# Kernel optimization log

Measured on AMD Instinct MI355X. Metric: run time of the kernel, lower is better.

## Reference

```python
import jax, jax.numpy as jnp
import numpy as np

D_MODEL = 1024
D_STATE = 16
D_CONV = 4
EXPAND = 2
D_INNER = EXPAND * D_MODEL          # 2048
DT_RANK = (D_MODEL + 15) // 16      # 64
B_SZ, SEQ = 2, 1024
LN_EPS = 1e-6


def setup_inputs() -> dict:
    key = jax.random.key(0)
    ks = jax.random.split(key, 12)
    s = 0.02
    x = jax.random.normal(ks[0], (B_SZ, SEQ, D_MODEL), dtype=jnp.float32)
    W_in = jax.random.normal(ks[1], (D_MODEL, 2 * D_INNER), dtype=jnp.float32) * s
    conv_w = jax.random.normal(ks[2], (D_INNER, D_CONV), dtype=jnp.float32) * s
    conv_b = jnp.zeros((D_INNER,), dtype=jnp.float32)
    W_xproj = jax.random.normal(ks[3], (D_INNER, DT_RANK + 2 * D_STATE), dtype=jnp.float32) * s
    W_dt = jax.random.normal(ks[4], (DT_RANK, D_INNER), dtype=jnp.float32) * (DT_RANK ** -0.5)
    # dt bias ~ log-uniform init as in Mamba (softplus^-1 of dt in [1e-3, 1e-1])
    dt = jnp.exp(jax.random.uniform(ks[5], (D_INNER,)) * (np.log(0.1) - np.log(1e-3)) + np.log(1e-3))
    b_dt = dt + jnp.log(-jnp.expm1(-dt))  # inverse softplus
    A_log = jnp.log(jnp.broadcast_to(jnp.arange(1, D_STATE + 1, dtype=jnp.float32), (D_INNER, D_STATE)))
    D_param = jnp.ones((D_INNER,), dtype=jnp.float32)
    W_out = jax.random.normal(ks[6], (D_INNER, D_MODEL), dtype=jnp.float32) * s
    gamma = jnp.ones((D_MODEL,), dtype=jnp.float32)
    beta = jnp.zeros((D_MODEL,), dtype=jnp.float32)
    return {"x": x, "W_in": W_in, "conv_w": conv_w, "conv_b": conv_b,
            "W_xproj": W_xproj, "W_dt": W_dt, "b_dt": b_dt, "A_log": A_log,
            "D_param": D_param, "W_out": W_out, "gamma": gamma, "beta": beta}


def _mamba(x, W_in, conv_w, conv_b, W_xproj, W_dt, b_dt, A_log, D_param, W_out):
    B, L, _ = x.shape
    xz = x @ W_in                                  # [B,L,2*d_inner]
    xi, z = jnp.split(xz, 2, axis=-1)              # [B,L,d_inner] each
    # causal depthwise conv1d, kernel D_CONV
    xp = jnp.pad(xi, ((0, 0), (D_CONV - 1, 0), (0, 0)))
    xc = conv_b
    for k in range(D_CONV):
        xc = xc + xp[:, k:k + L, :] * conv_w[:, k]
    xc = jax.nn.silu(xc)                           # [B,L,d_inner]
    x_dbl = xc @ W_xproj                           # [B,L,dt_rank+2*d_state]
    dt_r = x_dbl[..., :DT_RANK]
    B_ssm = x_dbl[..., DT_RANK:DT_RANK + D_STATE]  # [B,L,d_state]
    C_ssm = x_dbl[..., DT_RANK + D_STATE:]         # [B,L,d_state]
    dt = jax.nn.softplus(dt_r @ W_dt + b_dt)       # [B,L,d_inner]
    A = -jnp.exp(A_log)                            # [d_inner,d_state]
    dA = jnp.exp(dt[..., None] * A)                # [B,L,d_inner,d_state]
    dBu = dt[..., None] * B_ssm[:, :, None, :] * xc[..., None]
    # selective scan over time (time-major for lax.scan)
    dA_t = jnp.moveaxis(dA, 1, 0)                  # [L,B,d_inner,d_state]
    dBu_t = jnp.moveaxis(dBu, 1, 0)
    C_t = jnp.moveaxis(C_ssm, 1, 0)                # [L,B,d_state]
    h0 = jnp.zeros((B, D_INNER, D_STATE), dtype=x.dtype)

    def step(h, inp):
        a, bu, c = inp
        h = a * h + bu
        y = jnp.einsum('bdn,bn->bd', h, c)
        return h, y

    _, ys = jax.lax.scan(step, h0, (dA_t, dBu_t, C_t))
    y = jnp.moveaxis(ys, 0, 1)                     # [B,L,d_inner]
    y = y + xc * D_param
    y = y * jax.nn.silu(z)
    return y @ W_out                               # [B,L,d_model]


def reference(x, W_in, conv_w, conv_b, W_xproj, W_dt, b_dt, A_log, D_param, W_out, gamma, beta):
    m = _mamba(x, W_in, conv_w, conv_b, W_xproj, W_dt, b_dt, A_log, D_param, W_out)
    mu = jnp.mean(m, axis=-1, keepdims=True)
    var = jnp.mean(jnp.square(m - mu), axis=-1, keepdims=True)
    ln = (m - mu) * jax.lax.rsqrt(var + LN_EPS) * gamma + beta
    return x + ln
```

## Files before the change

### kernel.cpp

```cpp
#include <hip/hip_runtime.h>
#include <math.h>

#define DM   1024
#define DI   2048
#define DS   16
#define DTR  64
#define NB   2
#define SEQL 1024
#define NTOK (NB*SEQL)
#define XND  96
#define XNP  128
#define CK   128
#define CL   8
#define NPART 2

typedef __bf16 bf16x8 __attribute__((ext_vector_type(8)));
typedef __bf16 bf16x4 __attribute__((ext_vector_type(4)));
typedef float  f32x4  __attribute__((ext_vector_type(4)));

#define PREP_BLOCKS 3872

__device__ inline void trans_tile64(const float* __restrict__ W,
                                    __bf16* __restrict__ WT, int K, int N,
                                    int n0, int k0, int tid, __bf16 (*t)[65])
{
    const int tx = tid & 63, ty = tid >> 6;
    #pragma unroll
    for (int i = 0; i < 16; i++)
        t[ty * 16 + i][tx] = (__bf16)W[(size_t)(k0 + ty * 16 + i) * N + n0 + tx];
    __syncthreads();
    #pragma unroll
    for (int i = 0; i < 16; i++)
        WT[(size_t)(n0 + ty * 16 + i) * K + k0 + tx] = t[tx][ty * 16 + i];
}

__global__ __launch_bounds__(256) void prep(
    const float* __restrict__ x, const float* __restrict__ W_in,
    const float* __restrict__ W_out, const float* __restrict__ W_dt,
    const float* __restrict__ W_xprj,
    __bf16* __restrict__ xb, __bf16* __restrict__ W_inT,
    __bf16* __restrict__ W_outT, __bf16* __restrict__ WdtT,
    __bf16* __restrict__ W_xprT, float* __restrict__ xdbl)
{
    __shared__ __bf16 t[64][65];
    int bid = blockIdx.x;
    const int tid = threadIdx.x;

    if (bid < 256) {
        const int i = bid * 1024 + tid * 4;
        const float4 z = {0.f, 0.f, 0.f, 0.f};
        *reinterpret_cast<float4*>(&xdbl[i]) = z;
        return;
    }
    bid -= 256;
    if (bid < 1024) {
        const int e = (bid * 256 + tid) * 8;
        const float4 v0 = *reinterpret_cast<const float4*>(&x[e]);
        const float4 v1 = *reinterpret_cast<const float4*>(&x[e + 4]);
        bf16x8 o;
        o[0] = (__bf16)v0.x; o[1] = (__bf16)v0.y; o[2] = (__bf16)v0.z; o[3] = (__bf16)v0.w;
        o[4] = (__bf16)v1.x; o[5] = (__bf16)v1.y; o[6] = (__bf16)v1.z; o[7] = (__bf16)v1.w;
        *reinterpret_cast<bf16x8*>(&xb[e]) = o;
        return;
    }
    bid -= 1024;
    if (bid < 1024) {
        trans_tile64(W_in, W_inT, DM, 2 * DI, (bid & 63) * 64, (bid >> 6) * 64, tid, t);
        return;
    }
    bid -= 1024;
    if (bid < 512) {
        trans_tile64(W_out, W_outT, DI, DM, (bid & 15) * 64, (bid >> 4) * 64, tid, t);
        return;
    }
    bid -= 512;
    if (bid < 32) {
        trans_tile64(W_dt, WdtT, DTR, DI, bid * 64, 0, tid, t);
        return;
    }
    bid -= 32;
    {
        const int idx = bid * 256 + tid;
        const int k = idx & (DI - 1);
        const int n = idx >> 11;
        W_xprT[(size_t)n * DI + k] = (n < XND) ? (__bf16)W_xprj[(size_t)k * XND + n]
                                               : (__bf16)0.f;
    }
}

template<int MODE, int SWZ, int TN>
__global__ __launch_bounds__(256) void gemm_bf16(
    const __bf16* __restrict__ A, const __bf16* __restrict__ Bt,
    void* __restrict__ Cp, int M, int N, int K, int ldc,
    const float* __restrict__ bias)
{
    constexpr int NFR = TN / 32;
    constexpr bool PIPE = (MODE != 2);
    constexpr int ASZ = 128 * 64, BSZ = TN * 64;
    constexpr int STG = (PIPE ? 2 : 1) * (ASZ + BSZ);
    constexpr int SMEM = (STG > 128 * TN) ? STG : 128 * TN;
    __shared__ __bf16 smem[SMEM];
    const int tid  = threadIdx.x;
    const int lane = tid & 63;
    const int wid  = tid >> 6;
    const int wr   = wid >> 1, wc = wid & 1;

    int bx = blockIdx.x, by = blockIdx.y;
    if (SWZ == 1 || SWZ == 2) {
        const int gx = gridDim.x, gy = gridDim.y;
        const int nxy = gx * gy;
        const int q = nxy >> 3;
        int lin = by * gx + bx;
        lin = (lin & 7) * q + (lin >> 3);
        if (SWZ == 1) { by = lin / gx; bx = lin % gx; }
        else          { bx = lin / gy; by = lin % gy; }
    } else if (SWZ == 3) {
        const int lin = by * gridDim.x + bx;
        const int r   = lin & 7;
        const int idx = lin >> 3;
        bx = (r & 3) * 8 + (idx & 7);
        by = (r >> 2) * 8 + (idx >> 3);
    }
    const int brow = by * 128, bcol = bx * TN;
    const int kper = K / gridDim.z;
    const int kbeg = blockIdx.z * kper, kend = kbeg + kper;

    f32x4 acc[4][NFR] = {};

    auto stage = [&](int buf, int k0) {
        __bf16* As = smem + buf * (ASZ + BSZ);
        __bf16* Bs = As + ASZ;
        if (MODE == 2) {
            const float* Af = reinterpret_cast<const float*>(A);
            #pragma unroll
            for (int p = 0; p < 4; p++) {
                const int i = p * 256 + tid;
                const int r = i >> 3;
                const int j = i & 7;
                const float4 v0 = *reinterpret_cast<const float4*>(
                    &Af[(size_t)(brow + r) * XNP + j * 8]);
                const float4 v1 = *reinterpret_cast<const float4*>(
                    &Af[(size_t)(brow + r) * XNP + j * 8 + 4]);
                bf16x8 o;
                o[0] = (__bf16)v0.x; o[1] = (__bf16)v0.y; o[2] = (__bf16)v0.z; o[3] = (__bf16)v0.w;
                o[4] = (__bf16)v1.x; o[5] = (__bf16)v1.y; o[6] = (__bf16)v1.z; o[7] = (__bf16)v1.w;
                *reinterpret_cast<bf16x8*>(&As[r * 64 + ((j ^ (r & 7))) * 8]) = o;
            }
        } else {
            #pragma unroll
            for (int p = 0; p < 4; p++) {
                const int i = p * 256 + tid;
                const int r = i >> 3;
                const int gc = ((i & 7) ^ (r & 7)) * 8;
                __builtin_amdgcn_global_load_lds(
                    (const __attribute__((address_space(1))) void*)(A + (size_t)(brow + r) * K + k0 + gc),
                    (__attribute__((address_space(3))) void*)(&As[i * 8]), 16, 0, 0);
            }
        }
        #pragma unroll
        for (int p = 0; p < TN / 32; p++) {
            const int i = p * 256 + tid;
            const int r = i >> 3;
            const int gc = ((i & 7) ^ (r & 7)) * 8;
            __builtin_amdgcn_global_load_lds(
                (const __attribute__((address_space(1))) void*)(Bt + (size_t)(bcol + r) * K + k0 + gc),
                (__attribute__((address_space(3))) void*)(&Bs[i * 8]), 16, 0, 0);
        }
    };

    auto compute = [&](int buf) {
        const __bf16* As = smem + buf * (ASZ + BSZ);
        const __bf16* Bs = As + ASZ;
        bf16x8 a[2][4], b[2][NFR];
        const int rA = wr * 64 + (lane & 15);
        const int rB = wc * (TN / 2) + (lane & 15);
        const int cq = lane >> 4;
        const int rx = lane & 7;
        #pragma unroll
        for (int ks = 0; ks < 2; ks++) {
            const int sl = ((ks * 4 + cq) ^ rx) * 8;
            #pragma unroll
            for (int m = 0; m < 4; m++)
                a[ks][m] = *reinterpret_cast<const bf16x8*>(&As[(rA + m * 16) * 64 + sl]);
            #pragma unroll
            for (int n = 0; n < NFR; n++)
                b[ks][n] = *reinterpret_cast<const bf16x8*>(&Bs[(rB + n * 16) * 64 + sl]);
        }
        __builtin_amdgcn_s_setprio(1);
        #pragma unroll
        for (int ks = 0; ks < 2; ks++)
            #pragma unroll
            for (int m = 0; m < 4; m++)
                #pragma unroll
                for (int n = 0; n < NFR; n++)
                    acc[m][n] = __builtin_amdgcn_mfma_f32_16x16x32_bf16(
                        a[ks][m], b[ks][n], acc[m][n], 0, 0, 0);
        __builtin_amdgcn_s_setprio(0);
    };

    const int nt = (kend - kbeg) >> 6;
    if constexpr (PIPE) {
        constexpr int LOADS = 4 + TN / 32;
        stage(0, kbeg);
        int cur = 0;
        for (int t = 0; t < nt; t++) {
            if (t + 1 < nt) {
                stage(cur ^ 1, kbeg + ((t + 1) << 6));
                asm volatile("s_waitcnt vmcnt(%0)" :: "n"(LOADS) : "memory");
            } else {
                asm volatile("s_waitcnt vmcnt(0)" ::: "memory");
            }
            __builtin_amdgcn_s_barrier();
            __builtin_amdgcn_sched_barrier(0);
            compute(cur);
            __builtin_amdgcn_sched_barrier(0);
            __builtin_amdgcn_s_barrier();
            cur ^= 1;
        }
    } else {
        for (int k0 = kbeg; k0 < kend; k0 += 64) {
            __syncthreads();
            stage(0, k0);
            __syncthreads();
            compute(0);
        }
    }

    const int crl = wr * 64 + (lane >> 4) * 4;
    const int ccl = wc * (TN / 2) + (lane & 15);

    if (MODE == 1) {
        #pragma unroll
        for (int m = 0; m < 4; m++)
            #pragma unroll
            for (int n = 0; n < NFR; n++) {
                const int col = bcol + ccl + n * 16;
                #pragma unroll
                for (int j = 0; j < 4; j++)
                    atomicAdd(&((float*)Cp)[(size_t)(brow + crl + m * 16 + j) * ldc + col],
                              acc[m][n][j]);
            }
    } else {
        __syncthreads();
        __bf16* Cs = smem;
        #pragma unroll
        for (int m = 0; m < 4; m++)
            #pragma unroll
            for (int n = 0; n < NFR; n++) {
                #pragma unroll
                for (int j = 0; j < 4; j++) {
                    float v = acc[m][n][j];
                    if (MODE == 2) {
                        v += bias[bcol + ccl + n * 16];
                        v = fmaxf(v, 0.f) + log1pf(__expf(-fabsf(v)));
                    }
                    Cs[(crl + m * 16 + j) * TN + ccl + n * 16] = (__bf16)v;
                }
            }
        __syncthreads();
        __bf16* Cb = (__bf16*)Cp +
            (size_t)blockIdx.z * ((MODE == 3) ? (size_t)M * ldc : 0);
        constexpr int CHUNKS = 128 * TN / 8;
        #pragma unroll
        for (int p = 0; p < CHUNKS / 256; p++) {
            const int i = p * 256 + tid;
            const int r = i / (TN / 8);
            const int cc = (i % (TN / 8)) * 8;
            *reinterpret_cast<bf16x8*>(&Cb[(size_t)(brow + r) * ldc + bcol + cc]) =
                *reinterpret_cast<const bf16x8*>(&Cs[r * TN + cc]);
        }
    }
}

__global__ __launch_bounds__(256) void conv_silu(
    const __bf16* __restrict__ xzb, const float* __restrict__ conv_w,
    const float* __restrict__ conv_b, __bf16* __restrict__ xcb)
{
    const int q  = gridDim.x >> 3;
    const int sb = (blockIdx.x & 7) * q + (blockIdx.x >> 3);
    const int g  = sb * 256 + threadIdx.x;
    const int d0 = (g & 255) * 8;
    const int tok = g >> 8;
    const int t   = tok & (SEQL - 1);

    float4 wv[8];
    #pragma unroll
    for (int j = 0; j < 8; j++)
        wv[j] = *reinterpret_cast<const float4*>(&conv_w[(d0 + j) * 4]);
    float acc[8];
    {
        const float4 b0 = *reinterpret_cast<const float4*>(&conv_b[d0]);
        const float4 b1 = *reinterpret_cast<const float4*>(&conv_b[d0 + 4]);
        acc[0] = b0.x; acc[1] = b0.y; acc[2] = b0.z; acc[3] = b0.w;
        acc[4] = b1.x; acc[5] = b1.y; acc[6] = b1.z; acc[7] = b1.w;
    }
    #pragma unroll
    for (int k = 0; k < 4; k++) {
        const int tt = t + k - 3;
        if (tt >= 0) {
            const bf16x8 v = *reinterpret_cast<const bf16x8*>(
                &xzb[(size_t)(tok + k - 3) * (2 * DI) + d0]);
            #pragma unroll
            for (int j = 0; j < 8; j++) {
                const float wk = (k == 0) ? wv[j].x : (k == 1) ? wv[j].y
                               : (k == 2) ? wv[j].z : wv[j].w;
                acc[j] += (float)v[j] * wk;
            }
        }
    }
    bf16x8 o;
    #pragma unroll
    for (int j = 0; j < 8; j++) {
        const float a = acc[j];
        o[j] = (__bf16)(a / (1.f + __expf(-a)));
    }
    *reinterpret_cast<bf16x8*>(&xcb[(size_t)g * 8]) = o;
}

__global__ __launch_bounds__(256) void scan_partial(
    const __bf16* __restrict__ xcb, const float* __restrict__ xdbl,
    const __bf16* __restrict__ dtb, const float* __restrict__ A_log,
    __bf16* __restrict__ hpart, float* __restrict__ sdtb)
{
    __shared__ float Bsh[CL][16];
    const int tid = threadIdx.x;
    const int d = blockIdx.x * 256 + tid;
    const int c = blockIdx.y, b = blockIdx.z;
    const size_t base = (size_t)b * SEQL + c * CL;
    {
        const int st = tid >> 4, sg = tid & 15;
        if (st < CL) Bsh[st][sg] = xdbl[(base + st) * XNP + DTR + sg];
    }
    float dtv[CL], xcv[CL];
    #pragma unroll
    for (int t = 0; t < CL; t++) {
        dtv[t] = (float)dtb[(base + t) * DI + d];
        xcv[t] = (float)xcb[(base + t) * DI + d];
    }
    float Av[16];
    #pragma unroll
    for (int i = 0; i < 4; i++) {
        const float4 v = *reinterpret_cast<const float4*>(&A_log[(size_t)d * 16 + i * 4]);
        Av[i*4+0] = -__expf(v.x); Av[i*4+1] = -__expf(v.y);
        Av[i*4+2] = -__expf(v.z); Av[i*4+3] = -__expf(v.w);
    }
    __syncthreads();
    float h[16] = {};
    float sdt = 0.f;
    #pragma unroll
    for (int t = 0; t < CL; t++) {
        sdt += dtv[t];
        const float dx = dtv[t] * xcv[t];
        #pragma unroll
        for (int n = 0; n < 16; n++)
            h[n] = __expf(dtv[t] * Av[n]) * h[n] + dx * Bsh[t][n];
    }
    const size_t ob = ((size_t)(b * CK + c) * DI + d) * 16;
    bf16x8 o0, o1;
    #pragma unroll
    for (int i = 0; i < 8; i++) { o0[i] = (__bf16)h[i]; o1[i] = (__bf16)h[i + 8]; }
    *reinterpret_cast<bf16x8*>(&hpart[ob])     = o0;
    *reinterpret_cast<bf16x8*>(&hpart[ob + 8]) = o1;
    sdtb[(size_t)(b * CK + c) * DI + d] = sdt;
}

__global__ __launch_bounds__(256) void scan_combine(
    const float* __restrict__ A_log, const float* __restrict__ sdtb,
    const __bf16* __restrict__ hpart, __bf16* __restrict__ hentry)
{
    const int idx = blockIdx.x * 256 + threadIdx.x;
    const int n = idx & 15;
    const int d = (idx >> 4) & (DI - 1);
    const int b = idx >> 15;
    const float A = -__expf(A_log[(size_t)d * 16 + n]);
    float h = 0.f;
    for (int cb = 0; cb < CK / 16; cb++) {
        float hl[16], sv[16];
        #pragma unroll
        for (int j = 0; j < 16; j++) {
            const int c = cb * 16 + j;
            hl[j] = (float)hpart[((size_t)(b * CK + c) * DI + d) * 16 + n];
            sv[j] = sdtb[(size_t)(b * CK + c) * DI + d];
        }
        #pragma unroll
        for (int j = 0; j < 16; j++) {
            const int c = cb * 16 + j;
            hentry[((size_t)(b * CK + c) * DI + d) * 16 + n] = (__bf16)h;
            h = __expf(A * sv[j]) * h + hl[j];
        }
    }
}

__global__ __launch_bounds__(256) void scan_final(
    const __bf16* __restrict__ xzb, const __bf16* __restrict__ xcb,
    const float* __restrict__ xdbl, const __bf16* __restrict__ dtb,
    const float* __restrict__ A_log, const float* __restrict__ Dp,
    const __bf16* __restrict__ hentry, __bf16* __restrict__ yb)
{
    __shared__ float Bsh[CL][16];
    __shared__ float Csh[CL][16];
    const int tid = threadIdx.x;
    const int d = blockIdx.x * 256 + tid;
    const int c = blockIdx.y, b = blockIdx.z;
    const size_t base = (size_t)b * SEQL + c * CL;
    {
        const int st = tid >> 4, sg = tid & 15;
        if (st < CL)
            Bsh[st][sg] = xdbl[(base + st) * XNP + DTR + sg];
        else if (st < 2 * CL)
            Csh[st - CL][sg] = xdbl[(base + st - CL) * XNP + DTR + DS + sg];
    }
    float dtv[CL], xcv[CL], zv[CL];
    #pragma unroll
    for (int t = 0; t < CL; t++) {
        dtv[t] = (float)dtb[(base + t) * DI + d];
        xcv[t] = (float)xcb[(base + t) * DI + d];
        zv[t]  = (float)xzb[(base + t) * (2 * DI) + DI + d];
    }
    float Av[16];
    #pragma unroll
    for (int i = 0; i < 4; i++) {
        const float4 v = *reinterpret_cast<const float4*>(&A_log[(size_t)d * 16 + i * 4]);
        Av[i*4+0] = -__expf(v.x); Av[i*4+1] = -__expf(v.y);
        Av[i*4+2] = -__expf(v.z); Av[i*4+3] = -__expf(v.w);
    }
    float h[16];
    const size_t ob = ((size_t)(b * CK + c) * DI + d) * 16;
    {
        const bf16x8 v0 = *reinterpret_cast<const bf16x8*>(&hentry[ob]);
        const bf16x8 v1 = *reinterpret_cast<const bf16x8*>(&hentry[ob + 8]);
        #pragma unroll
        for (int i = 0; i < 8; i++) { h[i] = (float)v0[i]; h[i + 8] = (float)v1[i]; }
    }
    const float Dv = Dp[d];
    __syncthreads();
    #pragma unroll
    for (int t = 0; t < CL; t++) {
        const float dx = dtv[t] * xcv[t];
        float y = 0.f;
        #pragma unroll
        for (int n = 0; n < 16; n++) {
            h[n] = __expf(dtv[t] * Av[n]) * h[n] + dx * Bsh[t][n];
            y += h[n] * Csh[t][n];
        }
        y += xcv[t] * Dv;
        y *= zv[t] / (1.f + __expf(-zv[t]));
        yb[(base + t) * DI + d] = (__bf16)y;
    }
}

__global__ __launch_bounds__(256) void ln_add(
    const float* __restrict__ x, const __bf16* __restrict__ mpart,
    const float* __restrict__ gamma, const float* __restrict__ beta,
    float* __restrict__ out)
{
    const int tok = blockIdx.x;
    const int tid = threadIdx.x;
    const int lane = tid & 63, wave = tid >> 6;
    __shared__ float red1[4], red2[4];
    __shared__ float stats[2];

    float4 v = {0.f, 0.f, 0.f, 0.f};
    #pragma unroll
    for (int p = 0; p < NPART; p++) {
        const bf16x4 mv = *reinterpret_cast<const bf16x4*>(
            &mpart[((size_t)p * NTOK + tok) * DM + tid * 4]);
        v.x += (float)mv[0]; v.y += (float)mv[1];
        v.z += (float)mv[2]; v.w += (float)mv[3];
    }
    float s1 = v.x + v.y + v.z + v.w;
    float s2 = v.x * v.x + v.y * v.y + v.z * v.z + v.w * v.w;
    #pragma unroll
    for (int o = 32; o > 0; o >>= 1) {
        s1 += __shfl_down(s1, o, 64);
        s2 += __shfl_down(s2, o, 64);
    }
    if (lane == 0) { red1[wave] = s1; red2[wave] = s2; }
    __syncthreads();
    if (tid == 0) {
        const float m1 = (red1[0] + red1[1] + red1[2] + red1[3]) * (1.f / DM);
        const float m2 = (red2[0] + red2[1] + red2[2] + red2[3]) * (1.f / DM);
        stats[0] = m1;
        stats[1] = rsqrtf(fmaxf(m2 - m1 * m1, 0.f) + 1e-6f);
    }
    __syncthreads();
    const float mu = stats[0];
    const float rs = stats[1];

    const float4 g  = reinterpret_cast<const float4*>(gamma)[tid];
    const float4 bb = reinterpret_cast<const float4*>(beta)[tid];
    const float4 xv = reinterpret_cast<const float4*>(&x[(size_t)tok * DM])[tid];
    float4 o;
    o.x = xv.x + (v.x - mu) * rs * g.x + bb.x;
    o.y = xv.y + (v.y - mu) * rs * g.y + bb.y;
    o.z = xv.z + (v.z - mu) * rs * g.z + bb.z;
    o.w = xv.w + (v.w - mu) * rs * g.w + bb.w;
    reinterpret_cast<float4*>(&out[(size_t)tok * DM])[tid] = o;
}

extern "C" void kernel_launch(void* const* d_in, const int* in_sizes, int n_in,
                              void* d_out, int out_size, void* d_ws, size_t ws_size,
                              hipStream_t stream)
{
    const float* x      = (const float*)d_in[0];
    const float* W_in   = (const float*)d_in[1];
    const float* conv_w = (const float*)d_in[2];
    const float* conv_b = (const float*)d_in[3];
    const float* W_xprj = (const float*)d_in[4];
    const float* W_dt   = (const float*)d_in[5];
    const float* b_dt   = (const float*)d_in[6];
    const float* A_log  = (const float*)d_in[7];
    const float* D_par  = (const float*)d_in[8];
    const float* W_out  = (const float*)d_in[9];
    const float* gamma  = (const float*)d_in[10];
    const float* beta   = (const float*)d_in[11];
    float* out = (float*)d_out;

    char* w = (char*)d_ws;
    __bf16* xzb    = (__bf16*)(w + 0);
    __bf16* xcb    = (__bf16*)(w + 16777216);
    float*  xdbl   = (float*) (w + 25165824);
    __bf16* dtb    = (__bf16*)(w + 26214400);
    __bf16* mpart  = (__bf16*)(w + 34603008);
    __bf16* hpart  = (__bf16*)(w + 51380224);
    __bf16* hentry = (__bf16*)(w + 68157440);
    float*  sdtb   = (float*) (w + 84934656);
    __bf16* xb     = (__bf16*)(w + 87031808);
    __bf16* W_inT  = (__bf16*)(w + 91226112);
    __bf16* W_outT = (__bf16*)(w + 99614720);
    __bf16* W_xprT = (__bf16*)(w + 103809024);
    __bf16* WdtT   = (__bf16*)(w + 104333312);
    __bf16* yb     = (__bf16*)(w + 104595456);

    prep<<<PREP_BLOCKS, 256, 0, stream>>>(
        x, W_in, W_out, W_dt, W_xprj, xb, W_inT, W_outT, WdtT, W_xprT, xdbl);

    gemm_bf16<3, 3, 128><<<dim3(32, 16, 1), 256, 0, stream>>>(
        xb, W_inT, xzb, NTOK, 2 * DI, DM, 2 * DI, nullptr);

    conv_silu<<<(NTOK * DI / 8) / 256, 256, 0, stream>>>(xzb, conv_w, conv_b, xcb);

    gemm_bf16<1, 0, 128><<<dim3(1, 16, 16), 256, 0, stream>>>(
        xcb, W_xprT, xdbl, NTOK, XNP, DI, XNP, nullptr);

    gemm_bf16<2, 0, 64><<<dim3(32, 16, 1), 256, 0, stream>>>(
        (const __bf16*)xdbl, WdtT, dtb, NTOK, DI, DTR, DI, b_dt);

    scan_partial<<<dim3(DI / 256, CK, NB), 256, 0, stream>>>(
        xcb, xdbl, dtb, A_log, hpart, sdtb);
    scan_combine<<<NB * DI * DS / 256, 256, 0, stream>>>(A_log, sdtb, hpart, hentry);
    scan_final<<<dim3(DI / 256, CK, NB), 256, 0, stream>>>(
        xzb, xcb, xdbl, dtb, A_log, D_par, hentry, yb);

    gemm_bf16<3, 1, 128><<<dim3(8, 16, NPART), 256, 0, stream>>>(
        yb, W_outT, mpart, NTOK, DM, DI, DM, nullptr);

    ln_add<<<NTOK, 256, 0, stream>>>(x, mpart, gamma, beta, out);
}
```

Before: 148.6 us.

## Fuse dt projection and softplus into scan kernels, drop separate dt GEMM

Removes the dedicated dt_proj GEMM (MODE 2) that wrote a bf16 dt tensor, and instead recomputes dt per token inside both scan_partial and scan_final. Each thread loads its 64-wide W_dt row into registers, the block stages the dt_rank slice of x_dbl into shared memory, and a 64-term dot product plus softplus runs inline. This removes one launch and the write and re-read of a [tokens, d_inner] dt tensor. The cost is the dt projection being done twice on CUDA cores instead of once on MFMA, plus extra register pressure.

```diff
diff --git a/kernel.cpp b/kernel.cpp
--- a/kernel.cpp
+++ b/kernel.cpp
@@ -95,9 +95,8 @@
     const float* __restrict__ bias)
 {
     constexpr int NFR = TN / 32;
-    constexpr bool PIPE = (MODE != 2);
     constexpr int ASZ = 128 * 64, BSZ = TN * 64;
-    constexpr int STG = (PIPE ? 2 : 1) * (ASZ + BSZ);
+    constexpr int STG = 2 * (ASZ + BSZ);
     constexpr int SMEM = (STG > 128 * TN) ? STG : 128 * TN;
     __shared__ __bf16 smem[SMEM];
     const int tid  = threadIdx.x;
@@ -130,32 +129,14 @@
     auto stage = [&](int buf, int k0) {
         __bf16* As = smem + buf * (ASZ + BSZ);
         __bf16* Bs = As + ASZ;
-        if (MODE == 2) {
-            const float* Af = reinterpret_cast<const float*>(A);
-            #pragma unroll
-            for (int p = 0; p < 4; p++) {
-                const int i = p * 256 + tid;
-                const int r = i >> 3;
-                const int j = i & 7;
-                const float4 v0 = *reinterpret_cast<const float4*>(
-                    &Af[(size_t)(brow + r) * XNP + j * 8]);
-                const float4 v1 = *reinterpret_cast<const float4*>(
-                    &Af[(size_t)(brow + r) * XNP + j * 8 + 4]);
-                bf16x8 o;
-                o[0] = (__bf16)v0.x; o[1] = (__bf16)v0.y; o[2] = (__bf16)v0.z; o[3] = (__bf16)v0.w;
-                o[4] = (__bf16)v1.x; o[5] = (__bf16)v1.y; o[6] = (__bf16)v1.z; o[7] = (__bf16)v1.w;
-                *reinterpret_cast<bf16x8*>(&As[r * 64 + ((j ^ (r & 7))) * 8]) = o;
-            }
-        } else {
-            #pragma unroll
-            for (int p = 0; p < 4; p++) {
-                const int i = p * 256 + tid;
-                const int r = i >> 3;
-                const int gc = ((i & 7) ^ (r & 7)) * 8;
-                __builtin_amdgcn_global_load_lds(
-                    (const __attribute__((address_space(1))) void*)(A + (size_t)(brow + r) * K + k0 + gc),
-                    (__attribute__((address_space(3))) void*)(&As[i * 8]), 16, 0, 0);
-            }
+        #pragma unroll
+        for (int p = 0; p < 4; p++) {
+            const int i = p * 256 + tid;
+            const int r = i >> 3;
+            const int gc = ((i & 7) ^ (r & 7)) * 8;
+            __builtin_amdgcn_global_load_lds(
+                (const __attribute__((address_space(1))) void*)(A + (size_t)(brow + r) * K + k0 + gc),
+                (__attribute__((address_space(3))) void*)(&As[i * 8]), 16, 0, 0);
         }
         #pragma unroll
         for (int p = 0; p < TN / 32; p++) {
@@ -199,7 +180,7 @@
     };
 
     const int nt = (kend - kbeg) >> 6;
-    if constexpr (PIPE) {
+    {
         constexpr int LOADS = 4 + TN / 32;
         stage(0, kbeg);
         int cur = 0;
@@ -217,13 +198,6 @@
             __builtin_amdgcn_s_barrier();
             cur ^= 1;
         }
-    } else {
-        for (int k0 = kbeg; k0 < kend; k0 += 64) {
-            __syncthreads();
-            stage(0, k0);
-            __syncthreads();
-            compute(0);
-        }
     }
 
     const int crl = wr * 64 + (lane >> 4) * 4;
@@ -246,20 +220,12 @@
         #pragma unroll
         for (int m = 0; m < 4; m++)
             #pragma unroll
-            for (int n = 0; n < NFR; n++) {
+            for (int n = 0; n < NFR; n++)
                 #pragma unroll
-                for (int j = 0; j < 4; j++) {
-                    float v = acc[m][n][j];
-                    if (MODE == 2) {
-                        v += bias[bcol + ccl + n * 16];
-                        v = fmaxf(v, 0.f) + log1pf(__expf(-fabsf(v)));
-                    }
-                    Cs[(crl + m * 16 + j) * TN + ccl + n * 16] = (__bf16)v;
-                }
-            }
+                for (int j = 0; j < 4; j++)
+                    Cs[(crl + m * 16 + j) * TN + ccl + n * 16] = (__bf16)acc[m][n][j];
         __syncthreads();
-        __bf16* Cb = (__bf16*)Cp +
-            (size_t)blockIdx.z * ((MODE == 3) ? (size_t)M * ldc : 0);
+        __bf16* Cb = (__bf16*)Cp + (size_t)blockIdx.z * (size_t)M * ldc;
         constexpr int CHUNKS = 128 * TN / 8;
         #pragma unroll
         for (int p = 0; p < CHUNKS / 256; p++) {
@@ -317,12 +283,35 @@
     *reinterpret_cast<bf16x8*>(&xcb[(size_t)g * 8]) = o;
 }
 
+__device__ inline void stage_dtr(const float* __restrict__ xdbl,
+                                 size_t base, int tid, float (*Rsh)[64])
+{
+    const int rr = tid >> 5;
+    const int rc = (tid & 31) * 2;
+    const float2 rv = *reinterpret_cast<const float2*>(&xdbl[(base + rr) * XNP + rc]);
+    Rsh[rr][rc] = rv.x; Rsh[rr][rc + 1] = rv.y;
+}
+
+__device__ inline float dt_dot(const float (*Rsh)[64], int t,
+                               const bf16x8* wv, float bdt)
+{
+    float dot = bdt;
+    #pragma unroll
+    for (int i = 0; i < 8; i++)
+        #pragma unroll
+        for (int j = 0; j < 8; j++)
+            dot += Rsh[t][i * 8 + j] * (float)wv[i][j];
+    return fmaxf(dot, 0.f) + log1pf(__expf(-fabsf(dot)));
+}
+
 __global__ __launch_bounds__(256) void scan_partial(
     const __bf16* __restrict__ xcb, const float* __restrict__ xdbl,
-    const __bf16* __restrict__ dtb, const float* __restrict__ A_log,
+    const __bf16* __restrict__ WdtT, const float* __restrict__ b_dt,
+    const float* __restrict__ A_log,
     __bf16* __restrict__ hpart, float* __restrict__ sdtb)
 {
     __shared__ float Bsh[CL][16];
+    __shared__ float Rsh[CL][64];
     const int tid = threadIdx.x;
     const int d = blockIdx.x * 256 + tid;
     const int c = blockIdx.y, b = blockIdx.z;
@@ -330,13 +319,17 @@
     {
         const int st = tid >> 4, sg = tid & 15;
         if (st < CL) Bsh[st][sg] = xdbl[(base + st) * XNP + DTR + sg];
-    }
-    float dtv[CL], xcv[CL];
-    #pragma unroll
-    for (int t = 0; t < CL; t++) {
-        dtv[t] = (float)dtb[(base + t) * DI + d];
+        stage_dtr(xdbl, base, tid, Rsh);
+    }
+    bf16x8 wv[8];
+    #pragma unroll
+    for (int i = 0; i < 8; i++)
+        wv[i] = *reinterpret_cast<const bf16x8*>(&WdtT[(size_t)d * DTR + i * 8]);
+    const float bdt = b_dt[d];
+    float xcv[CL];
+    #pragma unroll
+    for (int t = 0; t < CL; t++)
         xcv[t] = (float)xcb[(base + t) * DI + d];
-    }
     float Av[16];
     #pragma unroll
     for (int i = 0; i < 4; i++) {
@@ -349,11 +342,12 @@
     float sdt = 0.f;
     #pragma unroll
     for (int t = 0; t < CL; t++) {
-        sdt += dtv[t];
-        const float dx = dtv[t] * xcv[t];
+        const float dtv = dt_dot(Rsh, t, wv, bdt);
+        sdt += dtv;
+        const float dx = dtv * xcv[t];
         #pragma unroll
         for (int n = 0; n < 16; n++)
-            h[n] = __expf(dtv[t] * Av[n]) * h[n] + dx * Bsh[t][n];
+            h[n] = __expf(dtv * Av[n]) * h[n] + dx * Bsh[t][n];
     }
     const size_t ob = ((size_t)(b * CK + c) * DI + d) * 16;
     bf16x8 o0, o1;
@@ -393,12 +387,14 @@
 
 __global__ __launch_bounds__(256) void scan_final(
     const __bf16* __restrict__ xzb, const __bf16* __restrict__ xcb,
-    const float* __restrict__ xdbl, const __bf16* __restrict__ dtb,
-    const float* __restrict__ A_log, const float* __restrict__ Dp,
-    const __bf16* __restrict__ hentry, __bf16* __restrict__ yb)
+    const float* __restrict__ xdbl, const __bf16* __restrict__ WdtT,
+    const float* __restrict__ b_dt, const float* __restrict__ A_log,
+    const float* __restrict__ Dp, const __bf16* __restrict__ hentry,
+    __bf16* __restrict__ yb)
 {
     __shared__ float Bsh[CL][16];
     __shared__ float Csh[CL][16];
+    __shared__ float Rsh[CL][64];
     const int tid = threadIdx.x;
     const int d = blockIdx.x * 256 + tid;
     const int c = blockIdx.y, b = blockIdx.z;
@@ -409,11 +405,16 @@
             Bsh[st][sg] = xdbl[(base + st) * XNP + DTR + sg];
         else if (st < 2 * CL)
             Csh[st - CL][sg] = xdbl[(base + st - CL) * XNP + DTR + DS + sg];
-    }
-    float dtv[CL], xcv[CL], zv[CL];
+        stage_dtr(xdbl, base, tid, Rsh);
+    }
+    bf16x8 wv[8];
+    #pragma unroll
+    for (int i = 0; i < 8; i++)
+        wv[i] = *reinterpret_cast<const bf16x8*>(&WdtT[(size_t)d * DTR + i * 8]);
+    const float bdt = b_dt[d];
+    float xcv[CL], zv[CL];
     #pragma unroll
     for (int t = 0; t < CL; t++) {
-        dtv[t] = (float)dtb[(base + t) * DI + d];
         xcv[t] = (float)xcb[(base + t) * DI + d];
         zv[t]  = (float)xzb[(base + t) * (2 * DI) + DI + d];
     }
@@ -436,11 +437,12 @@
     __syncthreads();
     #pragma unroll
     for (int t = 0; t < CL; t++) {
-        const float dx = dtv[t] * xcv[t];
+        const float dtv = dt_dot(Rsh, t, wv, bdt);
+        const float dx = dtv * xcv[t];
         float y = 0.f;
         #pragma unroll
         for (int n = 0; n < 16; n++) {
-            h[n] = __expf(dtv[t] * Av[n]) * h[n] + dx * Bsh[t][n];
+            h[n] = __expf(dtv * Av[n]) * h[n] + dx * Bsh[t][n];
             y += h[n] * Csh[t][n];
         }
         y += xcv[t] * Dv;
@@ -520,7 +522,6 @@
     __bf16* xzb    = (__bf16*)(w + 0);
     __bf16* xcb    = (__bf16*)(w + 16777216);
     float*  xdbl   = (float*) (w + 25165824);
-    __bf16* dtb    = (__bf16*)(w + 26214400);
     __bf16* mpart  = (__bf16*)(w + 34603008);
     __bf16* hpart  = (__bf16*)(w + 51380224);
     __bf16* hentry = (__bf16*)(w + 68157440);
@@ -543,14 +544,11 @@
     gemm_bf16<1, 0, 128><<<dim3(1, 16, 16), 256, 0, stream>>>(
         xcb, W_xprT, xdbl, NTOK, XNP, DI, XNP, nullptr);
 
-    gemm_bf16<2, 0, 64><<<dim3(32, 16, 1), 256, 0, stream>>>(
-        (const __bf16*)xdbl, WdtT, dtb, NTOK, DI, DTR, DI, b_dt);
-
     scan_partial<<<dim3(DI / 256, CK, NB), 256, 0, stream>>>(
-        xcb, xdbl, dtb, A_log, hpart, sdtb);
+        xcb, xdbl, WdtT, b_dt, A_log, hpart, sdtb);
     scan_combine<<<NB * DI * DS / 256, 256, 0, stream>>>(A_log, sdtb, hpart, hentry);
     scan_final<<<dim3(DI / 256, CK, NB), 256, 0, stream>>>(
-        xzb, xcb, xdbl, dtb, A_log, D_par, hentry, yb);
+        xzb, xcb, xdbl, WdtT, b_dt, A_log, D_par, hentry, yb);
 
     gemm_bf16<3, 1, 128><<<dim3(8, 16, NPART), 256, 0, stream>>>(
         yb, W_outT, mpart, NTOK, DM, DI, DM, nullptr);
```

Result: slower. 168.1 us (+13.1%).
